# Kernel optimization log

Hardware: AMD Instinct MI355X
Metric: run time of the kernel (lower is better)

## Reference

```python
import jax, jax.numpy as jnp
import numpy as np

BATCH, T, ALPHABET, N_STATES = 64, 4096, 32, 128


def setup_inputs() -> dict:
    key = jax.random.key(0)
    k1, k2, k3, k4 = jax.random.split(key, 4)
    # one-hot emission sequences (DNA-style categorical observations)
    tokens = jax.random.randint(k1, (BATCH, T), 0, ALPHABET)
    inputs = jax.nn.one_hot(tokens, ALPHABET, dtype=jnp.float32)  # [B, T, A]
    A_logits = jax.random.normal(k2, (N_STATES, N_STATES), dtype=jnp.float32)
    B_logits = jax.random.normal(k3, (ALPHABET, N_STATES), dtype=jnp.float32)
    I_logits = jax.random.normal(k4, (N_STATES,), dtype=jnp.float32)
    return {"inputs": inputs, "A_logits": A_logits, "B_logits": B_logits, "I_logits": I_logits}


def reference(inputs, A_logits, B_logits, I_logits):
    # Softmax-parameterized HMM: rows of A sum to 1 (transitions), columns of B
    # sum to 1 over the alphabet (emissions per state), I is the initial dist.
    A = jax.nn.softmax(A_logits, axis=1)          # [S, S]
    Bm = jax.nn.softmax(B_logits, axis=0)          # [A, S]
    I = jax.nn.softmax(I_logits)                   # [S]

    # Per-step emission likelihoods for every state (batched lookup via one-hot matmul)
    E = jnp.einsum('bta,as->bts', inputs, Bm)      # [B, T, S]

    # t = 0: alpha_0 = I * E_0, normalized; loglik accumulates the scale factors
    alpha = I[None, :] * E[:, 0]                   # [B, S]
    s = jnp.sum(alpha, axis=1, keepdims=True)      # [B, 1]
    alpha = alpha / s
    loglik = jnp.log(s[:, 0])                      # [B]

    def step(carry, Et):
        alpha, loglik = carry
        alpha = jnp.matmul(alpha, A) * Et          # [B, S]
        s = jnp.sum(alpha, axis=1, keepdims=True)
        alpha = alpha / s
        loglik = loglik + jnp.log(s[:, 0])
        return (alpha, loglik), None

    E_rest = jnp.swapaxes(E[:, 1:], 0, 1)          # time-major [T-1, B, S]
    (alpha, loglik), _ = jax.lax.scan(step, (alpha, loglik), E_rest)
    return loglik                                   # loglik_state, shape [B]
```

## Files before the change

kernel.cpp:

```cpp
#include <hip/hip_runtime.h>
#include <math.h>

#define BATCH 64
#define T 4096
#define ALPH 32
#define NS 128
#define MB 16
#define NGRP 4
#define NCHUNK 512
#define CL 8
#define WARM 16

typedef __bf16 bf16x8 __attribute__((ext_vector_type(8)));
typedef short  short8 __attribute__((ext_vector_type(8)));
typedef float  f32x4  __attribute__((ext_vector_type(4)));

#define WS_FRAG 0
#define WS_BME  8192
#define WS_I    10240
#define WS_TOK_F 10368

static __device__ inline unsigned short f2u(float f) {
    __bf16 b = (__bf16)f;
    return __builtin_bit_cast(unsigned short, b);
}


__global__ __launch_bounds__(256) void setup_kernel(const float* __restrict__ onehot,
                                                    const float* __restrict__ A_logits,
                                                    const float* __restrict__ B_logits,
                                                    const float* __restrict__ I_logits,
                                                    float* __restrict__ ws,
                                                    float* __restrict__ out,
                                                    unsigned char* __restrict__ tok) {
    unsigned short* frag = (unsigned short*)(ws + WS_FRAG);
    unsigned short* Bme  = (unsigned short*)(ws + WS_BME);
    float* I_ws = ws + WS_I;
    const int blk = blockIdx.x;
    const int tid = threadIdx.x;

    if (blk < 1024) {
        int b = blk >> 4;
        int t = (blk & 15) * 256 + tid;
        const float4* p = (const float4*)(onehot + ((size_t)b * T + t) * ALPH);
        int tk = 0;
        #pragma unroll
        for (int q = 0; q < 8; ++q) {
            float4 v = p[q];
            if (v.x > 0.5f) tk = 4 * q + 0;
            if (v.y > 0.5f) tk = 4 * q + 1;
            if (v.z > 0.5f) tk = 4 * q + 2;
            if (v.w > 0.5f) tk = 4 * q + 3;
        }
        tok[(size_t)b * T + t] = (unsigned char)tk;
        return;
    }

    if (blk == 1024 + NS) {
        if (tid < NS) {
            int s = tid;
            float m = -1e30f;
            for (int a = 0; a < ALPH; ++a) m = fmaxf(m, B_logits[a * NS + s]);
            float sum = 0.f;
            for (int a = 0; a < ALPH; ++a) sum += expf(B_logits[a * NS + s] - m);
            float inv = 1.0f / sum;
            int idx = (s & 15) * 8 + (s >> 4);
            for (int a = 0; a < ALPH; ++a)
                Bme[a * NS + idx] = f2u(expf(B_logits[a * NS + s] - m) * inv);
        } else if (tid < NS + BATCH) {
            out[tid - NS] = 0.0f;
        }
        __shared__ float redm[4];
        __shared__ float reds[4];
        float x = (tid < NS) ? I_logits[tid] : -1e30f;
        float m = x;
        #pragma unroll
        for (int off = 1; off < 64; off <<= 1) m = fmaxf(m, __shfl_xor(m, off));
        int wid = tid >> 6;
        if ((tid & 63) == 0) redm[wid] = m;
        __syncthreads();
        m = fmaxf(fmaxf(redm[0], redm[1]), fmaxf(redm[2], redm[3]));
        float e = (tid < NS) ? expf(x - m) : 0.0f;
        float sg = e;
        #pragma unroll
        for (int off = 1; off < 64; off <<= 1) sg += __shfl_xor(sg, off);
        if ((tid & 63) == 0) reds[wid] = sg;
        __syncthreads();
        float total = (reds[0] + reds[1]) + (reds[2] + reds[3]);
        if (tid < NS) {
            int n = tid;
            int p = (n >> 5) * 32 + (n & 15) * 2 + ((n >> 4) & 1);
            I_ws[p] = e / total;
        }
        return;
    }

    int rho = blk - 1024;
    __shared__ float redm[4];
    __shared__ float reds[4];
    float x = (tid < NS) ? A_logits[rho * NS + tid] : -1e30f;
    float m = x;
    #pragma unroll
    for (int off = 1; off < 64; off <<= 1) m = fmaxf(m, __shfl_xor(m, off));
    int wid = tid >> 6;
    if ((tid & 63) == 0) redm[wid] = m;
    __syncthreads();
    m = fmaxf(fmaxf(redm[0], redm[1]), fmaxf(redm[2], redm[3]));
    float e = (tid < NS) ? expf(x - m) : 0.0f;
    float sg = e;
    #pragma unroll
    for (int off = 1; off < 64; off <<= 1) sg += __shfl_xor(sg, off);
    if ((tid & 63) == 0) reds[wid] = sg;
    __syncthreads();
    float total = (reds[0] + reds[1]) + (reds[2] + reds[3]);
    if (tid < NS) {
        float v = e / total;
        int gamma = tid;
        int kc   = rho >> 5;
        int jlow = (rho >> 4) & 1;
        int quad = (rho >> 2) & 3;
        int j    = (rho & 3) * 2 + jlow;
        int nt   = gamma >> 4;
        int col  = gamma & 15;
        int lane = quad * 16 + col;
        int fid  = kc * 8 + nt;
        frag[fid * 512 + lane * 8 + j] = f2u(v);
    }
}

__global__ __launch_bounds__(256, 2) void hmm_kernel(const float* __restrict__ ws,
                                                     const unsigned char* __restrict__ tok_g,
                                                     float* __restrict__ out) {
    const unsigned short* Bme_g = (const unsigned short*)(ws + WS_BME);
    const float* I_ws = ws + WS_I;
    const char* frag_g = (const char*)(ws + WS_FRAG);

    const int c    = blockIdx.x;
    const int tid  = threadIdx.x;
    const int g    = tid >> 6;
    const int lane = tid & 63;
    const int quad = lane >> 4;
    const int col  = lane & 15;

    __shared__ unsigned short Bme_lds[ALPH * NS];
    __shared__ __align__(16) short alpha_lds[NGRP][MB * 136];
    __shared__ unsigned char tok_lds[(CL + WARM) * BATCH];

    const int t0u    = c * CL - WARM;
    const int t0     = (t0u < 0) ? 0 : t0u;
    const bool exact = (t0 == 0);
    const int nsteps = (c + 1) * CL - 1 - t0;
    const int ntok   = nsteps + 1;
    const int resetj = c * CL - t0;

    {
        const unsigned* src = (const unsigned*)Bme_g;
        unsigned* dst = (unsigned*)Bme_lds;
        #pragma unroll
        for (int i = 0; i < 8; ++i) dst[i * 256 + tid] = src[i * 256 + tid];
    }
    {
        int b = tid & 63, half = tid >> 6;
        if (half * 8 < ntok) {
            uint2 v = *(const uint2*)(tok_g + (size_t)b * T + t0 + half * 8);
            unsigned lo = v.x, hi = v.y;
            #pragma unroll
            for (int i = 0; i < 4; ++i) {
                tok_lds[(half * 8 + i) * 64 + b]     = (unsigned char)((lo >> (8 * i)) & 255);
                tok_lds[(half * 8 + 4 + i) * 64 + b] = (unsigned char)((hi >> (8 * i)) & 255);
            }
        }
    }
    bf16x8 bfr[32];
    #pragma unroll
    for (int fid = 0; fid < 32; ++fid)
        bfr[fid] = __builtin_bit_cast(bf16x8, *(const short8*)(frag_g + fid * 1024 + lane * 16));

    __syncthreads();

    {
        #pragma unroll
        for (int it = 0; it < 32; ++it) {
            int idx = it * 64 + lane;
            int m = idx >> 7, p = idx & 127;
            float val;
            if (exact) {
                int tk0 = tok_lds[0 * 64 + g * 16 + m];
                int nt = ((p >> 5) << 1) + (p & 1);
                int cc = (p >> 1) & 15;
                float bm = (float)__builtin_bit_cast(__bf16, Bme_lds[tk0 * NS + cc * 8 + nt]);
                val = I_ws[p] * bm;
            } else {
                val = 1.0f;
            }
            alpha_lds[g][m * 136 + p] = (short)f2u(val);
        }
    }

    float loglik = 0.0f;

    for (int j = 1; j <= nsteps; ++j) {
        const bool do_norm = ((j & 7) == 0) || (j == resetj);

        unsigned tokp = *(const unsigned*)&tok_lds[j * 64 + g * 16 + quad * 4];
        bf16x8 efr[4];
        #pragma unroll
        for (int r = 0; r < 4; ++r) {
            int tk = (tokp >> (8 * r)) & 255;
            efr[r] = *(const bf16x8*)&Bme_lds[tk * NS + col * 8];
        }

        const short* ap = &alpha_lds[g][col * 136 + quad * 8];
        bf16x8 afr[4];
        #pragma unroll
        for (int kc = 0; kc < 4; ++kc)
            afr[kc] = *(const bf16x8*)(ap + kc * 32);

        f32x4 acc[8];
        #pragma unroll
        for (int nt = 0; nt < 8; ++nt) acc[nt] = (f32x4){0.f, 0.f, 0.f, 0.f};
        #pragma unroll
        for (int nt = 0; nt < 8; ++nt) {
            #pragma unroll
            for (int kc = 0; kc < 4; ++kc)
                acc[nt] = __builtin_amdgcn_mfma_f32_16x16x32_bf16(afr[kc], bfr[kc * 8 + nt], acc[nt], 0, 0, 0);
        }

        float vv[4][8];
        #pragma unroll
        for (int r = 0; r < 4; ++r) {
            #pragma unroll
            for (int i = 0; i < 8; ++i)
                vv[r][i] = acc[i][r] * (float)efr[r][i];
        }

        if (do_norm) {
            float asum = 0.f;
            #pragma unroll
            for (int kc = 0; kc < 4; ++kc) {
                #pragma unroll
                for (int jj = 0; jj < 8; ++jj) asum += (float)afr[kc][jj];
            }
            asum += __shfl_xor(asum, 16);
            asum += __shfl_xor(asum, 32);
            float lg = __logf(asum);
            loglik = (j == resetj) ? 0.0f : (loglik + lg);
            #pragma unroll
            for (int r = 0; r < 4; ++r) {
                float iv = __builtin_amdgcn_rcpf(__shfl(asum, quad * 4 + r));
                #pragma unroll
                for (int i = 0; i < 8; ++i) vv[r][i] *= iv;
            }
        }

        #pragma unroll
        for (int r = 0; r < 4; ++r) {
            unsigned* wrow = (unsigned*)&alpha_lds[g][(quad * 4 + r) * 136];
            #pragma unroll
            for (int a = 0; a < 4; ++a) {
                unsigned u0 = __builtin_bit_cast(unsigned, vv[r][2 * a])     + 0x8000u;
                unsigned u1 = __builtin_bit_cast(unsigned, vv[r][2 * a + 1]) + 0x8000u;
                wrow[a * 16 + col] = __builtin_amdgcn_perm(u1, u0, 0x07060302u);
            }
        }
    }

    {
        const short* ap = &alpha_lds[g][col * 136 + quad * 8];
        float tot = 0.f;
        #pragma unroll
        for (int kc = 0; kc < 4; ++kc) {
            bf16x8 av = *(const bf16x8*)(ap + kc * 32);
            #pragma unroll
            for (int jj = 0; jj < 8; ++jj) tot += (float)av[jj];
        }
        tot += __shfl_xor(tot, 16);
        tot += __shfl_xor(tot, 32);
        if (quad == 0)
            atomicAdd(out + g * 16 + col, loglik + __logf(tot));
    }
}

extern "C" void kernel_launch(void* const* d_in, const int* in_sizes, int n_in,
                              void* d_out, int out_size, void* d_ws, size_t ws_size,
                              hipStream_t stream) {
    const float* onehot   = (const float*)d_in[0];
    const float* A_logits = (const float*)d_in[1];
    const float* B_logits = (const float*)d_in[2];
    const float* I_logits = (const float*)d_in[3];
    float* ws  = (float*)d_ws;
    float* out = (float*)d_out;
    unsigned char* tok = (unsigned char*)(ws + WS_TOK_F);

    setup_kernel<<<dim3(1024 + NS + 1), dim3(256), 0, stream>>>(
        onehot, A_logits, B_logits, I_logits, ws, out, tok);
    hmm_kernel<<<dim3(NCHUNK), dim3(256), 0, stream>>>(ws, tok, out);
}
```

Baseline: 112.9 us.

## Split each batch group's state columns across four waves with double-buffered alpha

Each block now handles one 16-sequence batch group for one time chunk. The block's four waves each compute 32 of the 128 output states, in place of one wave per group computing all 128 states. Alpha is double-buffered in LDS and a block-wide barrier runs each step. Chunk length doubles to 16 with half as many chunks, which cuts the share of warm-up steps that are redundant. The aim is shorter per-step critical paths and lower register pressure so four blocks fit per CU, at the cost of a __syncthreads every step. The special normalization at the reset step was dropped, so the loglik reset now depends only on the every-8-steps normalization lining up with resetj.

```diff
diff --git a/kernel.cpp b/kernel.cpp
--- a/kernel.cpp
+++ b/kernel.cpp
@@ -7,8 +7,8 @@
 #define NS 128
 #define MB 16
 #define NGRP 4
-#define NCHUNK 512
-#define CL 8
+#define NCHUNK 256
+#define CL 16
 #define WARM 16
 
 typedef __bf16 bf16x8 __attribute__((ext_vector_type(8)));
@@ -128,23 +128,24 @@
     }
 }
 
-__global__ __launch_bounds__(256, 2) void hmm_kernel(const float* __restrict__ ws,
+__global__ __launch_bounds__(256, 4) void hmm_kernel(const float* __restrict__ ws,
                                                      const unsigned char* __restrict__ tok_g,
                                                      float* __restrict__ out) {
     const unsigned short* Bme_g = (const unsigned short*)(ws + WS_BME);
     const float* I_ws = ws + WS_I;
-    const char* frag_g = (const char*)(ws + WS_FRAG);
-
-    const int c    = blockIdx.x;
+    const unsigned short* frag_g = (const unsigned short*)(ws + WS_FRAG);
+
+    const int g    = blockIdx.x;
+    const int c    = blockIdx.y;
     const int tid  = threadIdx.x;
-    const int g    = tid >> 6;
+    const int w    = tid >> 6;
     const int lane = tid & 63;
     const int quad = lane >> 4;
     const int col  = lane & 15;
 
     __shared__ unsigned short Bme_lds[ALPH * NS];
-    __shared__ __align__(16) short alpha_lds[NGRP][MB * 136];
-    __shared__ unsigned char tok_lds[(CL + WARM) * BATCH];
+    __shared__ __align__(16) short alpha_lds[2][MB * 136];
+    __shared__ unsigned char tok_lds[(CL + WARM) * MB];
 
     const int t0u    = c * CL - WARM;
     const int t0     = (t0u < 0) ? 0 : t0u;
@@ -159,88 +160,81 @@
         #pragma unroll
         for (int i = 0; i < 8; ++i) dst[i * 256 + tid] = src[i * 256 + tid];
     }
-    {
-        int b = tid & 63, half = tid >> 6;
-        if (half * 8 < ntok) {
-            uint2 v = *(const uint2*)(tok_g + (size_t)b * T + t0 + half * 8);
-            unsigned lo = v.x, hi = v.y;
-            #pragma unroll
-            for (int i = 0; i < 4; ++i) {
-                tok_lds[(half * 8 + i) * 64 + b]     = (unsigned char)((lo >> (8 * i)) & 255);
-                tok_lds[(half * 8 + 4 + i) * 64 + b] = (unsigned char)((hi >> (8 * i)) & 255);
-            }
-        }
-    }
-    bf16x8 bfr[32];
-    #pragma unroll
-    for (int fid = 0; fid < 32; ++fid)
-        bfr[fid] = __builtin_bit_cast(bf16x8, *(const short8*)(frag_g + fid * 1024 + lane * 16));
-
-    __syncthreads();
-
-    {
-        #pragma unroll
-        for (int it = 0; it < 32; ++it) {
-            int idx = it * 64 + lane;
-            int m = idx >> 7, p = idx & 127;
-            float val;
-            if (exact) {
-                int tk0 = tok_lds[0 * 64 + g * 16 + m];
-                int nt = ((p >> 5) << 1) + (p & 1);
-                int cc = (p >> 1) & 15;
-                float bm = (float)__builtin_bit_cast(__bf16, Bme_lds[tk0 * NS + cc * 8 + nt]);
-                val = I_ws[p] * bm;
-            } else {
-                val = 1.0f;
-            }
-            alpha_lds[g][m * 136 + p] = (short)f2u(val);
-        }
-    }
+    for (int i = tid; i < ntok * MB; i += 256)
+        tok_lds[i] = tok_g[(size_t)(g * MB + (i & 15)) * T + t0 + (i >> 4)];
+
+    bf16x8 bfr[4][2];
+    #pragma unroll
+    for (int kc = 0; kc < 4; ++kc)
+        #pragma unroll
+        for (int b = 0; b < 2; ++b)
+            bfr[kc][b] = __builtin_bit_cast(bf16x8,
+                *(const short8*)(frag_g + (size_t)(kc * 8 + 2 * w + b) * 512 + lane * 8));
+
+    __syncthreads();
+
+    #pragma unroll
+    for (int it = 0; it < 8; ++it) {
+        int idx = it * 256 + tid;
+        int m = idx >> 7, p = idx & 127;
+        float val;
+        if (exact) {
+            int tk0 = tok_lds[m];
+            int nt = ((p >> 5) << 1) + (p & 1);
+            int cc = (p >> 1) & 15;
+            float bm = (float)__builtin_bit_cast(__bf16, Bme_lds[tk0 * NS + cc * 8 + nt]);
+            val = I_ws[p] * bm;
+        } else {
+            val = 1.0f;
+        }
+        alpha_lds[0][m * 136 + p] = (short)f2u(val);
+    }
+    __syncthreads();
 
     float loglik = 0.0f;
 
     for (int j = 1; j <= nsteps; ++j) {
-        const bool do_norm = ((j & 7) == 0) || (j == resetj);
-
-        unsigned tokp = *(const unsigned*)&tok_lds[j * 64 + g * 16 + quad * 4];
-        bf16x8 efr[4];
+        const int rb = (j + 1) & 1;
+        const int wb = j & 1;
+        const bool do_norm = ((j & 7) == 0);
+
+        unsigned tokp = *(const unsigned*)&tok_lds[j * MB + quad * 4];
+        unsigned eu[4];
         #pragma unroll
         for (int r = 0; r < 4; ++r) {
             int tk = (tokp >> (8 * r)) & 255;
-            efr[r] = *(const bf16x8*)&Bme_lds[tk * NS + col * 8];
-        }
-
-        const short* ap = &alpha_lds[g][col * 136 + quad * 8];
+            eu[r] = *(const unsigned*)&Bme_lds[tk * NS + col * 8 + 2 * w];
+        }
+
+        const short* ap = &alpha_lds[rb][col * 136 + quad * 8];
         bf16x8 afr[4];
         #pragma unroll
         for (int kc = 0; kc < 4; ++kc)
             afr[kc] = *(const bf16x8*)(ap + kc * 32);
 
-        f32x4 acc[8];
-        #pragma unroll
-        for (int nt = 0; nt < 8; ++nt) acc[nt] = (f32x4){0.f, 0.f, 0.f, 0.f};
-        #pragma unroll
-        for (int nt = 0; nt < 8; ++nt) {
-            #pragma unroll
-            for (int kc = 0; kc < 4; ++kc)
-                acc[nt] = __builtin_amdgcn_mfma_f32_16x16x32_bf16(afr[kc], bfr[kc * 8 + nt], acc[nt], 0, 0, 0);
-        }
-
-        float vv[4][8];
+        f32x4 acc0 = {0.f, 0.f, 0.f, 0.f};
+        f32x4 acc1 = {0.f, 0.f, 0.f, 0.f};
+        #pragma unroll
+        for (int kc = 0; kc < 4; ++kc) {
+            acc0 = __builtin_amdgcn_mfma_f32_16x16x32_bf16(afr[kc], bfr[kc][0], acc0, 0, 0, 0);
+            acc1 = __builtin_amdgcn_mfma_f32_16x16x32_bf16(afr[kc], bfr[kc][1], acc1, 0, 0, 0);
+        }
+
+        float v0[4], v1[4];
         #pragma unroll
         for (int r = 0; r < 4; ++r) {
-            #pragma unroll
-            for (int i = 0; i < 8; ++i)
-                vv[r][i] = acc[i][r] * (float)efr[r][i];
+            float e0 = __builtin_bit_cast(float, eu[r] << 16);
+            float e1 = __builtin_bit_cast(float, eu[r] & 0xffff0000u);
+            v0[r] = acc0[r] * e0;
+            v1[r] = acc1[r] * e1;
         }
 
         if (do_norm) {
             float asum = 0.f;
             #pragma unroll
-            for (int kc = 0; kc < 4; ++kc) {
+            for (int kc = 0; kc < 4; ++kc)
                 #pragma unroll
                 for (int jj = 0; jj < 8; ++jj) asum += (float)afr[kc][jj];
-            }
             asum += __shfl_xor(asum, 16);
             asum += __shfl_xor(asum, 32);
             float lg = __logf(asum);
@@ -248,25 +242,23 @@
             #pragma unroll
             for (int r = 0; r < 4; ++r) {
                 float iv = __builtin_amdgcn_rcpf(__shfl(asum, quad * 4 + r));
-                #pragma unroll
-                for (int i = 0; i < 8; ++i) vv[r][i] *= iv;
+                v0[r] *= iv;
+                v1[r] *= iv;
             }
         }
 
         #pragma unroll
         for (int r = 0; r < 4; ++r) {
-            unsigned* wrow = (unsigned*)&alpha_lds[g][(quad * 4 + r) * 136];
-            #pragma unroll
-            for (int a = 0; a < 4; ++a) {
-                unsigned u0 = __builtin_bit_cast(unsigned, vv[r][2 * a])     + 0x8000u;
-                unsigned u1 = __builtin_bit_cast(unsigned, vv[r][2 * a + 1]) + 0x8000u;
-                wrow[a * 16 + col] = __builtin_amdgcn_perm(u1, u0, 0x07060302u);
-            }
-        }
+            unsigned u0 = __builtin_bit_cast(unsigned, v0[r]) + 0x8000u;
+            unsigned u1 = __builtin_bit_cast(unsigned, v1[r]) + 0x8000u;
+            unsigned dw = __builtin_amdgcn_perm(u1, u0, 0x07060302u);
+            ((unsigned*)&alpha_lds[wb][0])[(quad * 4 + r) * 68 + w * 16 + col] = dw;
+        }
+        __syncthreads();
     }
 
     {
-        const short* ap = &alpha_lds[g][col * 136 + quad * 8];
+        const short* ap = &alpha_lds[nsteps & 1][col * 136 + quad * 8];
         float tot = 0.f;
         #pragma unroll
         for (int kc = 0; kc < 4; ++kc) {
@@ -276,8 +268,8 @@
         }
         tot += __shfl_xor(tot, 16);
         tot += __shfl_xor(tot, 32);
-        if (quad == 0)
-            atomicAdd(out + g * 16 + col, loglik + __logf(tot));
+        if (w == 0 && quad == 0)
+            atomicAdd(out + g * MB + col, loglik + __logf(tot));
     }
 }
 
@@ -294,5 +286,5 @@
 
     setup_kernel<<<dim3(1024 + NS + 1), dim3(256), 0, stream>>>(
         onehot, A_logits, B_logits, I_logits, ws, out, tok);
-    hmm_kernel<<<dim3(NCHUNK), dim3(256), 0, stream>>>(ws, tok, out);
-}
+    hmm_kernel<<<dim3(NGRP, NCHUNK), dim3(256), 0, stream>>>(ws, tok, out);
+}
```

Result: faster. 105.6 us (-6.4%).
